# Kernel optimization log

Measured on AMD Instinct MI355X. Metric: run time of the kernel, lower is better.

The kernel has to match this reference:

```python
import jax, jax.numpy as jnp
import numpy as np

B, S, D, H = 2, 2048, 4096, 32
Dh = D // H          # 128, rotary_dim == head_dim
BASE = 10000.0       # rope_theta
SCALE = Dh ** -0.5


def setup_inputs() -> dict:
    key = jax.random.key(0)
    k0, k1, k2 = jax.random.split(key, 3)
    w_scale = 0.02
    return {
        "hidden_states": jax.random.normal(k0, (B, S, D), jnp.float32),
        "positions": jnp.broadcast_to(jnp.arange(S, dtype=jnp.int32), (B, S)),
        "Wqkv": jax.random.normal(k1, (D, 3 * D), jnp.float32) * w_scale,
        "bqkv": jnp.zeros((3 * D,), jnp.float32),
        "Wproj": jax.random.normal(k2, (D, D), jnp.float32) * w_scale,
    }


def _apply_rope(x, positions):
    # x: [B, S, H, Dh]; neox-style (rotate-half) RoPE, as in vLLM PagedAttentionWithRoPE
    half = Dh // 2
    inv_freq = 1.0 / (BASE ** (jnp.arange(half, dtype=jnp.float32) / half))
    ang = positions[..., None].astype(jnp.float32) * inv_freq      # [B, S, half]
    cos = jnp.cos(ang)[:, :, None, :]                              # [B, S, 1, half]
    sin = jnp.sin(ang)[:, :, None, :]
    x1, x2 = x[..., :half], x[..., half:]
    return jnp.concatenate([x1 * cos - x2 * sin, x2 * cos + x1 * sin], axis=-1)


def reference(hidden_states, positions, Wqkv, bqkv, Wproj):
    # c_attn: fused QKV projection
    qkv = hidden_states @ Wqkv + bqkv                              # [B, S, 3D]
    q, k, v = jnp.split(qkv, 3, axis=-1)
    q = q.reshape(B, S, H, Dh)
    k = k.reshape(B, S, H, Dh)
    v = v.reshape(B, S, H, Dh)
    # fused RoPE on q and k at the given positions
    q = _apply_rope(q, positions)
    k = _apply_rope(k, positions)
    # causal scaled-dot-product attention (prefill semantics of paged attention)
    scores = jnp.einsum("bqhd,bkhd->bhqk", q, k) * SCALE           # [B, H, S, S]
    causal = jnp.tril(jnp.ones((S, S), dtype=bool))
    scores = jnp.where(causal, scores, jnp.finfo(scores.dtype).min)
    attn = jax.nn.softmax(scores, axis=-1)
    ctx = jnp.einsum("bhqk,bkhd->bqhd", attn, v).reshape(B, S, D)
    # c_proj (no bias)
    return ctx @ Wproj
```

## Files before the change

### kernel.cpp

```cpp
#include <hip/hip_runtime.h>

typedef __attribute__((ext_vector_type(8))) short short8;
typedef __attribute__((ext_vector_type(4))) short short4v;
typedef __attribute__((ext_vector_type(4))) float f32x4;

#define LDS8(base, off) (*(const short8*)((const char*)(base) + (off)))
#define GLOAD_LDS16(gp, lp) __builtin_amdgcn_global_load_lds( \
    (const __attribute__((address_space(1))) unsigned int*)(gp), \
    (__attribute__((address_space(3))) unsigned int*)(lp), 16, 0, 0)
#define SBAR() __builtin_amdgcn_s_barrier()
#define SB0() __builtin_amdgcn_sched_barrier(0)

__device__ __forceinline__ short f2bf(float f) {
    unsigned u = __builtin_bit_cast(unsigned, f);
    unsigned r = (u + 0x7FFFu + ((u >> 16) & 1u)) >> 16;
    return (short)r;
}
__device__ __forceinline__ float bf2f(short s) {
    unsigned u = ((unsigned)(unsigned short)s) << 16;
    return __builtin_bit_cast(float, u);
}

__global__ __launch_bounds__(256) void cvt_f32_bf16(const float* __restrict__ in,
                                                    short* __restrict__ out, int n8) {
    int i = blockIdx.x * 256 + threadIdx.x;
    if (i < n8) {
        const f32x4* p = (const f32x4*)(in + (size_t)i * 8);
        f32x4 a = p[0], bq = p[1];
        short8 o;
        o[0] = f2bf(a[0]); o[1] = f2bf(a[1]); o[2] = f2bf(a[2]); o[3] = f2bf(a[3]);
        o[4] = f2bf(bq[0]); o[5] = f2bf(bq[1]); o[6] = f2bf(bq[2]); o[7] = f2bf(bq[3]);
        *(short8*)(out + (size_t)i * 8) = o;
    }
}

__global__ __launch_bounds__(256) void transpose_cvt(const float* __restrict__ W,
                                                     short* __restrict__ Out, int R, int C) {
    __shared__ float tile[64][33];
    int c0 = blockIdx.x * 64, r0 = blockIdx.y * 32;
    int tid = threadIdx.x;
    int cc4 = (tid & 15) * 4;
#pragma unroll
    for (int it = 0; it < 2; ++it) {
        int rr = (tid >> 4) + it * 16;
        f32x4 v = *(const f32x4*)&W[(size_t)(r0 + rr) * C + c0 + cc4];
#pragma unroll
        for (int i = 0; i < 4; ++i) tile[cc4 + i][rr] = v[i];
    }
    __syncthreads();
    int cc = tid >> 2, r8 = (tid & 3) * 8;
    short8 o;
#pragma unroll
    for (int i = 0; i < 8; ++i) o[i] = f2bf(tile[cc][r8 + i]);
    *(short8*)&Out[(size_t)(c0 + cc) * R + r0 + r8] = o;
}

__global__ __launch_bounds__(256) void rope_table(float* __restrict__ ctab, float* __restrict__ stab) {
    int idx = blockIdx.x * 256 + threadIdx.x;
    int t = idx >> 6, j = idx & 63;
    float inv = expf(-(float)j * (9.210340371976184f / 64.0f));
    float ang = (float)t * inv;
    ctab[idx] = cosf(ang);
    stab[idx] = sinf(ang);
}

__global__ __launch_bounds__(256) void rope_scatter(const short* __restrict__ qkv,
                                                    const int* __restrict__ pos,
                                                    const float* __restrict__ ctab,
                                                    const float* __restrict__ stab,
                                                    short* __restrict__ Q, short* __restrict__ K) {
    int id = blockIdx.x * 256 + threadIdx.x;
    int j = id & 63;
    int h = (id >> 6) & 31;
    int s = (id >> 11) & 2047;
    int b = id >> 22;
    size_t qrow = (size_t)(b * 2048 + s) * 12288 + h * 128;
    float q1 = bf2f(qkv[qrow + j]),        q2 = bf2f(qkv[qrow + 64 + j]);
    float k1 = bf2f(qkv[qrow + 4096 + j]), k2 = bf2f(qkv[qrow + 4160 + j]);
    int p = pos[b * 2048 + s];
    float c = ctab[p * 64 + j], si = stab[p * 64 + j];
    size_t orow = ((size_t)(b * 32 + h) * 2048 + s) * 128;
    Q[orow + j]      = f2bf(q1 * c - q2 * si);
    Q[orow + 64 + j] = f2bf(q2 * c + q1 * si);
    K[orow + j]      = f2bf(k1 * c - k2 * si);
    K[orow + 64 + j] = f2bf(k2 * c + k1 * si);
}

__global__ __launch_bounds__(256) void v_transpose(const short* __restrict__ qkv,
                                                   short* __restrict__ Vt) {
    int bh = blockIdx.z; int b = bh >> 5, h = bh & 31;
    int s0 = blockIdx.x * 64, d0 = blockIdx.y * 64;
    __shared__ short tile[64][65];
    int tid = threadIdx.x;
    int sl = tid >> 3;
    int d8 = (tid & 7) * 8;
#pragma unroll
    for (int it = 0; it < 2; ++it) {
        int s = sl + it * 32;
        short8 v = *(const short8*)&qkv[(size_t)(b * 2048 + s0 + s) * 12288 + 8192 + h * 128 + d0 + d8];
#pragma unroll
        for (int i = 0; i < 8; ++i) tile[s][d8 + i] = v[i];
    }
    __syncthreads();
    int dl = tid >> 3;
    int s8 = (tid & 7) * 8;
#pragma unroll
    for (int it = 0; it < 2; ++it) {
        int d = dl + it * 32;
        short8 o;
#pragma unroll
        for (int i = 0; i < 8; ++i) o[i] = tile[s8 + i][d];
        *(short8*)&Vt[((size_t)bh * 128 + d0 + d) * 2048 + s0 + s8] = o;
    }
}

__global__ __launch_bounds__(512, 2) void gemm256(const short* __restrict__ A,
                                                  const short* __restrict__ Bt,
                                                  const float* __restrict__ bias,
                                                  short* __restrict__ Cbf,
                                                  float* __restrict__ Cf,
                                                  int M, int N, int K, int nN) {
    __shared__ __align__(16) char smem[131072];
    const int tid = threadIdx.x;
    const int l = tid & 63, w = tid >> 6;
    const int m = l & 15, g = l >> 4, m7 = m & 7;
    const int wm = w >> 2, wn = w & 3;

    int cpx = gridDim.x >> 3;
    int wg = (blockIdx.x & 7) * cpx + (blockIdx.x >> 3);
    int gsz = nN << 3;
    int grp = wg / gsz, rem = wg - grp * gsz;
    int bm = (grp << 3) + (rem & 7);
    int bn = rem >> 3;
    int m0 = bm << 8, n0 = bn << 8;

    const int srow = l >> 3;
    const int sgcol = ((l & 7) ^ srow) << 3;
    const int NT = K >> 6;

    const int AbaseR = wm << 14;
    const int BbaseR = 32768 + ((wn >> 1) << 14);
    const int brow0 = (wn & 1) << 6;

    f32x4 acc[8][4];
    const f32x4 fz = {0.f, 0.f, 0.f, 0.f};
#pragma unroll
    for (int i = 0; i < 8; ++i)
#pragma unroll
        for (int j = 0; j < 4; ++j) acc[i][j] = fz;

    auto stage_half = [&](const short* G, int grow0, int kcol, int ldsoff) {
        GLOAD_LDS16(G + (size_t)(grow0 +      w * 8 + srow) * K + kcol + sgcol,
                    smem + ldsoff + w * 1024);
        GLOAD_LDS16(G + (size_t)(grow0 + 64 + w * 8 + srow) * K + kcol + sgcol,
                    smem + ldsoff + 8192 + w * 1024);
    };

    short8 afX[2][2], afY[2][2], bf[4][2];

#define RD_AF(DST, BASE, I0)                                                     \
    _Pragma("unroll")                                                            \
    for (int i2 = 0; i2 < 2; ++i2) {                                             \
        _Pragma("unroll")                                                        \
        for (int kk = 0; kk < 2; ++kk)                                           \
            DST[i2][kk] = LDS8(BASE, (((I0) + i2) * 16 + m) * 128 + (((kk * 4 + g) ^ m7) << 4)); \
    }
#define RD_BF(BASE)                                                              \
    _Pragma("unroll")                                                            \
    for (int j2 = 0; j2 < 4; ++j2) {                                             \
        _Pragma("unroll")                                                        \
        for (int kk = 0; kk < 2; ++kk)                                           \
            bf[j2][kk] = LDS8(BASE, (brow0 + j2 * 16 + m) * 128 + (((kk * 4 + g) ^ m7) << 4)); \
    }
#define MFMA_IP(IP, AF)                                                          \
    do {                                                                         \
        __builtin_amdgcn_s_setprio(1);                                           \
        _Pragma("unroll")                                                        \
        for (int kk = 0; kk < 2; ++kk) {                                         \
            _Pragma("unroll")                                                    \
            for (int i2 = 0; i2 < 2; ++i2) {                                     \
                _Pragma("unroll")                                                \
                for (int j2 = 0; j2 < 4; ++j2) {                                 \
                    acc[(IP) * 2 + i2][j2] = __builtin_amdgcn_mfma_f32_16x16x32_bf16( \
                        AF[i2][kk], bf[j2][kk], acc[(IP) * 2 + i2][j2], 0, 0, 0); \
                }                                                                \
            }                                                                    \
        }                                                                        \
        __builtin_amdgcn_s_setprio(0);                                           \
    } while (0)

#pragma unroll
    for (int t = 0; t < 2; ++t) {
        int sb = t << 16;
        stage_half(A,  m0,       t * 64, sb);
        stage_half(A,  m0 + 128, t * 64, sb + 16384);
        stage_half(Bt, n0,       t * 64, sb + 32768);
        stage_half(Bt, n0 + 128, t * 64, sb + 49152);
    }
    asm volatile("s_waitcnt vmcnt(8)");
    SB0();
    SBAR();
    {
        const char* Ab0 = smem + AbaseR;
        const char* Bb0 = smem + BbaseR;
        RD_BF(Bb0);
        RD_AF(afX, Ab0, 0);
        SB0();
    }

    for (int kt = 0; kt < NT; ++kt) {
        const int slotb  = (kt & 1) << 16;
        const int slotbN = ((kt + 1) & 1) << 16;
        const char* Ab  = smem + slotb + AbaseR;
        const char* AbN = smem + slotbN + AbaseR;
        const char* BbN = smem + slotbN + BbaseR;
        const bool nx = (kt + 1) < NT;
        const bool pf = (kt + 2) < NT;
        const int kc = (kt + 2) << 6;

        RD_AF(afY, Ab, 2); SB0();
        asm volatile("s_waitcnt lgkmcnt(4)"); SB0();
        MFMA_IP(0, afX);
        RD_AF(afX, Ab, 4); SB0();
        asm volatile("s_waitcnt lgkmcnt(4)"); SB0();
        MFMA_IP(1, afY);
        RD_AF(afY, Ab, 6); SB0();
        asm volatile("s_waitcnt lgkmcnt(4)"); SB0();
        MFMA_IP(2, afX);
        asm volatile("s_waitcnt lgkmcnt(0)"); SB0();
        asm volatile("s_waitcnt vmcnt(0)"); SB0();
        SBAR();
        MFMA_IP(3, afY);
        if (nx) {
            RD_BF(BbN); SB0();
            RD_AF(afX, AbN, 0); SB0();
            if (pf) {
                stage_half(A,  m0,       kc, slotb);
                stage_half(A,  m0 + 128, kc, slotb + 16384);
                stage_half(Bt, n0,       kc, slotb + 32768);
                stage_half(Bt, n0 + 128, kc, slotb + 49152);
            }
        }
    }
#undef RD_AF
#undef RD_BF
#undef MFMA_IP

#pragma unroll
    for (int i = 0; i < 8; ++i) {
#pragma unroll
        for (int j = 0; j < 4; ++j) {
#pragma unroll
            for (int r = 0; r < 4; ++r) {
                int row = m0 + wm * 128 + i * 16 + g * 4 + r;
                int col = n0 + wn * 64 + j * 16 + m;
                float v = acc[i][j][r];
                if (bias) v += bias[col];
                if (Cbf) Cbf[(size_t)row * N + col] = f2bf(v);
                else     Cf[(size_t)row * N + col] = v;
            }
        }
    }
}

__global__ __launch_bounds__(512, 4) void flash_fwd(const short* __restrict__ Q,
                                                    const short* __restrict__ Kt,
                                                    const short* __restrict__ Vt,
                                                    short* __restrict__ ctx) {
    const int S = 2048;
    const float SCALE = 0.08838834764831845f;
    __shared__ __align__(16) char smem[65536];

    int tid = threadIdx.x, l = tid & 63, w = tid >> 6;
    int m = l & 15, g = l >> 4, m7 = m & 7;
    int qg = blockIdx.x, h = blockIdx.y, b = blockIdx.z;
    int bh = b * 32 + h;
    int q0 = qg * 128 + w * 16;

    const short* Qg = Q + ((size_t)bh * S + q0) * 128;
    const short* Kg = Kt + (size_t)bh * S * 128;
    const short* Vg = Vt + (size_t)bh * 128 * S;

    short8 qf[4];
#pragma unroll
    for (int kb = 0; kb < 4; ++kb)
        qf[kb] = *(const short8*)(Qg + m * 128 + kb * 32 + g * 8);

    const f32x4 fz = {0.f, 0.f, 0.f, 0.f};
    f32x4 O[8];
#pragma unroll
    for (int nb = 0; nb < 8; ++nb) O[nb] = fz;
    f32x4 La = fz;
    short8 ones;
#pragma unroll
    for (int i = 0; i < 8; ++i) ones[i] = (short)0x3F80;

    const short* Kp[2]; const short* Vp[2]; int KlO[2], VlO[2];
#pragma unroll
    for (int q = 0; q < 2; ++q) {
        int c = w * 2 + q;
        int rowK = c * 4 + (l >> 4);
        Kp[q] = Kg + (size_t)rowK * 128 + (((l & 15) ^ (rowK & 7)) * 8);
        KlO[q] = c * 1024;
        int rowV = c * 8 + (l >> 3);
        Vp[q] = Vg + (size_t)rowV * S + (((l & 7) ^ (rowV & 7)) * 8);
        VlO[q] = c * 1024;
    }

    auto stageK = [&](int t, int slot) {
#pragma unroll
        for (int q = 0; q < 2; ++q)
            GLOAD_LDS16(Kp[q] + (size_t)t * 8192, smem + slot * 16384 + KlO[q]);
    };
    auto stageV = [&](int t) {
#pragma unroll
        for (int q = 0; q < 2; ++q)
            GLOAD_LDS16(Vp[q] + t * 64, smem + 32768 + VlO[q]);
    };

    int nkt = 2 * qg + 2;
    stageK(0, 0);
    stageV(0);

    for (int kt = 0; kt < nkt; ++kt) {
        int slot = kt & 1;
        const char* Kl = smem + slot * 16384;
        const char* Vl = smem + 32768;
        char* Pl = smem + 49152 + w * 2048;
        int k0 = kt * 64;
        bool comp = (k0 <= q0 + 15);
        bool more = (kt + 1 < nkt);

        if (more) { stageK(kt + 1, slot ^ 1); asm volatile("s_waitcnt vmcnt(4)"); }
        else      {                           asm volatile("s_waitcnt vmcnt(2)"); }
        SB0();
        SBAR();
        if (comp) {
            f32x4 sc[4];
#pragma unroll
            for (int j = 0; j < 4; ++j) sc[j] = fz;
#pragma unroll
            for (int kb = 0; kb < 4; ++kb) {
#pragma unroll
                for (int j = 0; j < 4; ++j) {
                    short8 kf = LDS8(Kl, (j * 16 + m) * 256 + (((kb * 4 + g) ^ m7) << 4));
                    sc[j] = __builtin_amdgcn_mfma_f32_16x16x32_bf16(qf[kb], kf, sc[j], 0, 0, 0);
                }
            }
            bool diag = (k0 + 63 > q0);
#pragma unroll
            for (int r = 0; r < 4; ++r) {
                int qrow = q0 + g * 4 + r;
                float s0 = sc[0][r] * SCALE;
                float s1 = sc[1][r] * SCALE;
                float s2 = sc[2][r] * SCALE;
                float s3 = sc[3][r] * SCALE;
                if (diag) {
                    if (k0 + m > qrow)      s0 = -__builtin_inff();
                    if (k0 + 16 + m > qrow) s1 = -__builtin_inff();
                    if (k0 + 32 + m > qrow) s2 = -__builtin_inff();
                    if (k0 + 48 + m > qrow) s3 = -__builtin_inff();
                }
                float p0 = __expf(s0);
                float p1 = __expf(s1);
                float p2 = __expf(s2);
                float p3 = __expf(s3);
                int pr = g * 4 + r;
                char* pw = Pl + pr * 128;
                float pv[4] = {p0, p1, p2, p3};
#pragma unroll
                for (int j = 0; j < 4; ++j) {
                    int lb = j * 32 + m * 2;
                    int pb = (((lb >> 4) ^ (pr & 7)) << 4) | (lb & 15);
                    *(short*)(pw + pb) = f2bf(pv[j]);
                }
            }
        }
        if (more) asm volatile("s_waitcnt vmcnt(2)");
        else      asm volatile("s_waitcnt vmcnt(0)");
        SB0();
        SBAR();
        if (comp) {
            short8 pf[2];
#pragma unroll
            for (int kh = 0; kh < 2; ++kh)
                pf[kh] = LDS8(Pl, m * 128 + (((kh * 4 + g) ^ m7) << 4));
#pragma unroll
            for (int kh = 0; kh < 2; ++kh) {
                La = __builtin_amdgcn_mfma_f32_16x16x32_bf16(pf[kh], ones, La, 0, 0, 0);
#pragma unroll
                for (int nb = 0; nb < 8; ++nb) {
                    int d = nb * 16 + m;
                    short8 vf = LDS8(Vl, d * 128 + (((kh * 4 + g) ^ m7) << 4));
                    O[nb] = __builtin_amdgcn_mfma_f32_16x16x32_bf16(pf[kh], vf, O[nb], 0, 0, 0);
                }
            }
        }
        SBAR();
        if (more) stageV(kt + 1);
    }
#pragma unroll
    for (int nb = 0; nb < 8; ++nb) {
#pragma unroll
        for (int r = 0; r < 4; ++r) {
            int row = q0 + g * 4 + r;
            float v = O[nb][r] / La[r];
            ctx[(size_t)(b * S + row) * 4096 + h * 128 + nb * 16 + m] = f2bf(v);
        }
    }
}

extern "C" void kernel_launch(void* const* d_in, const int* in_sizes, int n_in,
                              void* d_out, int out_size, void* d_ws, size_t ws_size,
                              hipStream_t stream) {
    const float* hidden    = (const float*)d_in[0];
    const int*   positions = (const int*)d_in[1];
    const float* Wqkv      = (const float*)d_in[2];
    const float* bqkv      = (const float*)d_in[3];
    const float* Wproj     = (const float*)d_in[4];
    float* out = (float*)d_out;
    char* ws = (char*)d_ws;

    short* Abf    = (short*)(ws + 0ull);
    short* WqkvT  = (short*)(ws + 33554432ull);
    short* WprojT = (short*)(ws + 134217728ull);
    short* qkv    = (short*)(ws + 167772160ull);
    short* Qr     = (short*)(ws + 268435456ull);
    short* Kr     = (short*)(ws + 301989888ull);
    short* Vt     = (short*)(ws + 335544320ull);
    short* ctx    = (short*)(ws + 369098752ull);
    float* ctab   = (float*)(ws + 402653184ull);
    float* stab   = (float*)(ws + 403177472ull);

    cvt_f32_bf16<<<8192, 256, 0, stream>>>(hidden, Abf, 2097152);
    transpose_cvt<<<dim3(192, 128), 256, 0, stream>>>(Wqkv, WqkvT, 4096, 12288);
    transpose_cvt<<<dim3(64, 128), 256, 0, stream>>>(Wproj, WprojT, 4096, 4096);
    rope_table<<<512, 256, 0, stream>>>(ctab, stab);
    gemm256<<<dim3(768), 512, 0, stream>>>(Abf, WqkvT, bqkv, qkv, nullptr, 4096, 12288, 4096, 48);
    rope_scatter<<<32768, 256, 0, stream>>>(qkv, positions, ctab, stab, Qr, Kr);
    v_transpose<<<dim3(32, 2, 64), 256, 0, stream>>>(qkv, Vt);
    flash_fwd<<<dim3(16, 32, 2), 512, 0, stream>>>(Qr, Kr, Vt, ctx);
    gemm256<<<dim3(256), 512, 0, stream>>>(ctx, WprojT, nullptr, nullptr, out, 4096, 4096, 4096, 16);
}
```

Before: 817.8 us.

## Fuse RoPE and V transpose into QKV GEMM epilogue via permuted weight columns

Permutes the Q/K output columns of the transposed QKV weight so that each rotate-half pair lands in adjacent lanes. The QKV GEMM epilogue can then apply RoPE with a lane shuffle and write Q/K directly in head-major layout, and write V already transposed. This removes the intermediate qkv buffer round-trip and two separate kernels. The cost is scattered 2-byte stores and per-element position/table loads in the epilogue.

```diff
diff --git a/kernel.cpp b/kernel.cpp
--- a/kernel.cpp
+++ b/kernel.cpp
@@ -35,7 +35,8 @@
 }
 
 __global__ __launch_bounds__(256) void transpose_cvt(const float* __restrict__ W,
-                                                     short* __restrict__ Out, int R, int C) {
+                                                     short* __restrict__ Out, int R, int C,
+                                                     int permqk) {
     __shared__ float tile[64][33];
     int c0 = blockIdx.x * 64, r0 = blockIdx.y * 32;
     int tid = threadIdx.x;
@@ -52,7 +53,13 @@
     short8 o;
 #pragma unroll
     for (int i = 0; i < 8; ++i) o[i] = f2bf(tile[cc][r8 + i]);
-    *(short8*)&Out[(size_t)(c0 + cc) * R + r0 + r8] = o;
+    int orow = c0 + cc;
+    if (permqk && orow < 8192) {
+        int j = orow & 127;
+        int jp = (j < 64) ? (j << 1) : (((j - 64) << 1) | 1);
+        orow = (orow & ~127) | jp;
+    }
+    *(short8*)&Out[(size_t)orow * R + r0 + r8] = o;
 }
 
 __global__ __launch_bounds__(256) void rope_table(float* __restrict__ ctab, float* __restrict__ stab) {
@@ -64,62 +71,18 @@
     stab[idx] = sinf(ang);
 }
 
-__global__ __launch_bounds__(256) void rope_scatter(const short* __restrict__ qkv,
-                                                    const int* __restrict__ pos,
-                                                    const float* __restrict__ ctab,
-                                                    const float* __restrict__ stab,
-                                                    short* __restrict__ Q, short* __restrict__ K) {
-    int id = blockIdx.x * 256 + threadIdx.x;
-    int j = id & 63;
-    int h = (id >> 6) & 31;
-    int s = (id >> 11) & 2047;
-    int b = id >> 22;
-    size_t qrow = (size_t)(b * 2048 + s) * 12288 + h * 128;
-    float q1 = bf2f(qkv[qrow + j]),        q2 = bf2f(qkv[qrow + 64 + j]);
-    float k1 = bf2f(qkv[qrow + 4096 + j]), k2 = bf2f(qkv[qrow + 4160 + j]);
-    int p = pos[b * 2048 + s];
-    float c = ctab[p * 64 + j], si = stab[p * 64 + j];
-    size_t orow = ((size_t)(b * 32 + h) * 2048 + s) * 128;
-    Q[orow + j]      = f2bf(q1 * c - q2 * si);
-    Q[orow + 64 + j] = f2bf(q2 * c + q1 * si);
-    K[orow + j]      = f2bf(k1 * c - k2 * si);
-    K[orow + 64 + j] = f2bf(k2 * c + k1 * si);
-}
-
-__global__ __launch_bounds__(256) void v_transpose(const short* __restrict__ qkv,
-                                                   short* __restrict__ Vt) {
-    int bh = blockIdx.z; int b = bh >> 5, h = bh & 31;
-    int s0 = blockIdx.x * 64, d0 = blockIdx.y * 64;
-    __shared__ short tile[64][65];
-    int tid = threadIdx.x;
-    int sl = tid >> 3;
-    int d8 = (tid & 7) * 8;
-#pragma unroll
-    for (int it = 0; it < 2; ++it) {
-        int s = sl + it * 32;
-        short8 v = *(const short8*)&qkv[(size_t)(b * 2048 + s0 + s) * 12288 + 8192 + h * 128 + d0 + d8];
-#pragma unroll
-        for (int i = 0; i < 8; ++i) tile[s][d8 + i] = v[i];
-    }
-    __syncthreads();
-    int dl = tid >> 3;
-    int s8 = (tid & 7) * 8;
-#pragma unroll
-    for (int it = 0; it < 2; ++it) {
-        int d = dl + it * 32;
-        short8 o;
-#pragma unroll
-        for (int i = 0; i < 8; ++i) o[i] = tile[s8 + i][d];
-        *(short8*)&Vt[((size_t)bh * 128 + d0 + d) * 2048 + s0 + s8] = o;
-    }
-}
-
 __global__ __launch_bounds__(512, 2) void gemm256(const short* __restrict__ A,
                                                   const short* __restrict__ Bt,
                                                   const float* __restrict__ bias,
-                                                  short* __restrict__ Cbf,
                                                   float* __restrict__ Cf,
-                                                  int M, int N, int K, int nN) {
+                                                  int M, int N, int K, int nN,
+                                                  const int* __restrict__ pos,
+                                                  const float* __restrict__ ctab,
+                                                  const float* __restrict__ stab,
+                                                  short* __restrict__ Qr,
+                                                  short* __restrict__ Kr,
+                                                  short* __restrict__ Vtt,
+                                                  int mode) {
     __shared__ __align__(16) char smem[131072];
     const int tid = threadIdx.x;
     const int l = tid & 63, w = tid >> 6;
@@ -246,18 +209,66 @@
 #undef RD_BF
 #undef MFMA_IP
 
-#pragma unroll
-    for (int i = 0; i < 8; ++i) {
-#pragma unroll
-        for (int j = 0; j < 4; ++j) {
-#pragma unroll
-            for (int r = 0; r < 4; ++r) {
-                int row = m0 + wm * 128 + i * 16 + g * 4 + r;
+    if (mode == 0) {
+#pragma unroll
+        for (int i = 0; i < 8; ++i) {
+#pragma unroll
+            for (int j = 0; j < 4; ++j) {
+#pragma unroll
+                for (int r = 0; r < 4; ++r) {
+                    int row = m0 + wm * 128 + i * 16 + g * 4 + r;
+                    int col = n0 + wn * 64 + j * 16 + m;
+                    Cf[(size_t)row * N + col] = acc[i][j][r];
+                }
+            }
+        }
+        return;
+    }
+
+    int region = n0 >> 12;
+    if (region < 2) {
+        short* Dst = (region == 0) ? Qr : Kr;
+#pragma unroll
+        for (int i = 0; i < 8; ++i) {
+#pragma unroll
+            for (int j = 0; j < 4; ++j) {
                 int col = n0 + wn * 64 + j * 16 + m;
-                float v = acc[i][j][r];
-                if (bias) v += bias[col];
-                if (Cbf) Cbf[(size_t)row * N + col] = f2bf(v);
-                else     Cf[(size_t)row * N + col] = v;
+                int cr = col & 4095;
+                int hh = cr >> 7;
+                int jp = cr & 127;
+                int jj = jp >> 1;
+                int odd = jp & 1;
+                int jo = jj + (odd ? 64 : 0);
+                float bv = bias ? bias[region * 4096 + hh * 128 + jo] : 0.f;
+#pragma unroll
+                for (int r = 0; r < 4; ++r) {
+                    int row = m0 + wm * 128 + i * 16 + g * 4 + r;
+                    float v = acc[i][j][r] + bv;
+                    float partner = __shfl_xor(v, 1, 64);
+                    int p = pos[row];
+                    float c = ctab[p * 64 + jj], si = stab[p * 64 + jj];
+                    float outv = odd ? (v * c + partner * si) : (v * c - partner * si);
+                    int bI = row >> 11, s = row & 2047;
+                    Dst[((size_t)(bI * 32 + hh) * 2048 + s) * 128 + jo] = f2bf(outv);
+                }
+            }
+        }
+    } else {
+#pragma unroll
+        for (int i = 0; i < 8; ++i) {
+#pragma unroll
+            for (int j = 0; j < 4; ++j) {
+                int col = n0 + wn * 64 + j * 16 + m;
+                int cr = col & 4095;
+                int hh = cr >> 7;
+                int d = cr & 127;
+                float bv = bias ? bias[8192 + cr] : 0.f;
+                int row0 = m0 + wm * 128 + i * 16 + g * 4;
+                int bI = row0 >> 11, s0 = row0 & 2047;
+                short4v o4;
+#pragma unroll
+                for (int r = 0; r < 4; ++r) o4[r] = f2bf(acc[i][j][r] + bv);
+                *(short4v*)&Vtt[((size_t)(bI * 32 + hh) * 128 + d) * 2048 + s0] = o4;
             }
         }
     }
@@ -424,7 +435,6 @@
     short* Abf    = (short*)(ws + 0ull);
     short* WqkvT  = (short*)(ws + 33554432ull);
     short* WprojT = (short*)(ws + 134217728ull);
-    short* qkv    = (short*)(ws + 167772160ull);
     short* Qr     = (short*)(ws + 268435456ull);
     short* Kr     = (short*)(ws + 301989888ull);
     short* Vt     = (short*)(ws + 335544320ull);
@@ -433,12 +443,12 @@
     float* stab   = (float*)(ws + 403177472ull);
 
     cvt_f32_bf16<<<8192, 256, 0, stream>>>(hidden, Abf, 2097152);
-    transpose_cvt<<<dim3(192, 128), 256, 0, stream>>>(Wqkv, WqkvT, 4096, 12288);
-    transpose_cvt<<<dim3(64, 128), 256, 0, stream>>>(Wproj, WprojT, 4096, 4096);
+    transpose_cvt<<<dim3(192, 128), 256, 0, stream>>>(Wqkv, WqkvT, 4096, 12288, 1);
+    transpose_cvt<<<dim3(64, 128), 256, 0, stream>>>(Wproj, WprojT, 4096, 4096, 0);
     rope_table<<<512, 256, 0, stream>>>(ctab, stab);
-    gemm256<<<dim3(768), 512, 0, stream>>>(Abf, WqkvT, bqkv, qkv, nullptr, 4096, 12288, 4096, 48);
-    rope_scatter<<<32768, 256, 0, stream>>>(qkv, positions, ctab, stab, Qr, Kr);
-    v_transpose<<<dim3(32, 2, 64), 256, 0, stream>>>(qkv, Vt);
+    gemm256<<<dim3(768), 512, 0, stream>>>(Abf, WqkvT, bqkv, nullptr, 4096, 12288, 4096, 48,
+                                           positions, ctab, stab, Qr, Kr, Vt, 1);
     flash_fwd<<<dim3(16, 32, 2), 512, 0, stream>>>(Qr, Kr, Vt, ctx);
-    gemm256<<<dim3(256), 512, 0, stream>>>(ctx, WprojT, nullptr, nullptr, out, 4096, 4096, 4096, 16);
-}
+    gemm256<<<dim3(256), 512, 0, stream>>>(ctx, WprojT, nullptr, out, 4096, 4096, 4096, 16,
+                                           nullptr, nullptr, nullptr, nullptr, nullptr, nullptr, 0);
+}
```

Measured after the change: 757.5 us (median of 2 runs). -7.4%, faster.
